# Kernel optimization log

Measured on AMD Instinct MI355X. Metric: run time of the kernel, lower is better.

The kernel has to match this reference:

```python
import jax, jax.numpy as jnp
import numpy as np

B, S, D, H = 2, 1024, 768, 12
HD = D // H          # head_dim = 64
DFF = 4 * D          # 3072
EPS = 1e-5


def _ln(x, g, b):
    m = x.mean(-1, keepdims=True)
    v = ((x - m) ** 2).mean(-1, keepdims=True)
    return (x - m) * jax.lax.rsqrt(v + EPS) * g + b


def setup_inputs() -> dict:
    key = jax.random.key(0)
    ks = jax.random.split(key, 8)
    w = lambda k, shape: jax.random.normal(k, shape, jnp.float32) * 0.02
    return {
        "inp": jax.random.normal(ks[0], (B, S, D), jnp.float32),
        "attention_mask": jnp.zeros((B, S), bool),  # True = masked out (filled with -inf)
        "rel_matrix": jax.random.randint(ks[1], (B, S, S), -1, 2, jnp.int32),  # values in {-1,0,1}
        "qkv_w": w(ks[2], (3 * D, D)),
        "rel_A": w(ks[3], (3, HD)),        # relative_position_emb_A.weight
        "o_w": w(ks[4], (D, D)),
        "w1": w(ks[5], (DFF, D)), "b1": jnp.zeros((DFF,), jnp.float32),
        "w2": w(ks[6], (D, DFF)), "b2": jnp.zeros((D,), jnp.float32),
        "ln1_g": jnp.ones((D,), jnp.float32), "ln1_b": jnp.zeros((D,), jnp.float32),
        "ln2_g": jnp.ones((D,), jnp.float32), "ln2_b": jnp.zeros((D,), jnp.float32),
    }


def reference(inp, attention_mask, rel_matrix, qkv_w, rel_A, o_w,
              w1, b1, w2, b2, ln1_g, ln1_b, ln2_g, ln2_b):
    x = _ln(inp, ln1_g, ln1_b)
    qkv = x @ qkv_w.T                                  # (B,S,3D)
    q, k, v = jnp.split(qkv, 3, axis=-1)
    heads = lambda t: t.reshape(B, S, H, HD).transpose(0, 2, 1, 3)  # (B,H,S,HD)
    q, k, v = heads(q), heads(k), heads(v)

    # q @ (k + rel_emb)^T without materializing k_aug:
    # q.k^T term plus per-(q,key) relative term gathered from q @ A^T.
    logits = jnp.einsum("bhqd,bhkd->bhqk", q, k)       # (B,H,S,S)
    r = jnp.einsum("bhqd,cd->bhqc", q, rel_A)          # (B,H,S,3)
    idx = (rel_matrix + 1).astype(jnp.int32)           # (B,S,S) in {0,1,2}
    rel = jnp.take_along_axis(r, jnp.broadcast_to(idx[:, None], (B, H, S, S)), axis=-1)
    logits = (logits + rel) / np.sqrt(HD).astype(np.float32)
    # masked_fill: -inf where mask is True
    logits = jnp.where(attention_mask[:, None, None, :], -jnp.inf, logits)

    attn = jax.nn.softmax(logits, axis=-1)
    out = jnp.einsum("bhqk,bhkd->bhqd", attn, v)
    out = out.transpose(0, 2, 1, 3).reshape(B, S, D)
    inp = inp + out @ o_w.T                            # residual (dropout=0)

    h = _ln(inp, ln2_g, ln2_b)
    mlp = jax.nn.relu(h @ w1.T + b1) @ w2.T + b2
    return inp + mlp
```

## Files before the change

kernel.cpp:

```cpp
#include <hip/hip_runtime.h>
#include <hip/hip_bf16.h>

#define BB 2
#define SS 1024
#define DD 768
#define HH 12
#define HD 64
#define DFF 3072
#define EPS 1e-5f
#define BS2 (BB * SS)
#define BSD ((size_t)BS2 * DD)

typedef unsigned short ushort_t;
typedef unsigned char uchar_t;
using short8 = __attribute__((ext_vector_type(8))) short;
using f32x4  = __attribute__((ext_vector_type(4))) float;

__device__ __forceinline__ ushort_t f2bf_rne(float f) {
    union { float f; unsigned u; } x; x.f = f;
    unsigned r = x.u + 0x7fff + ((x.u >> 16) & 1);
    return (ushort_t)(r >> 16);
}
__device__ __forceinline__ float bf2f(short u) {
    union { unsigned i; float f; } x;
    x.i = ((unsigned)(ushort_t)u) << 16;
    return x.f;
}

__global__ __launch_bounds__(256) void cvt_bf16(
    const float* __restrict__ in, ushort_t* __restrict__ out, int n4)
{
    int i = blockIdx.x * 256 + threadIdx.x;
    if (i < n4) {
        float4 v = ((const float4*)in)[i];
        ushort4 o;
        o.x = f2bf_rne(v.x); o.y = f2bf_rne(v.y);
        o.z = f2bf_rne(v.z); o.w = f2bf_rne(v.w);
        ((ushort4*)out)[i] = o;
    }
}

__global__ __launch_bounds__(256) void build_codes(
    const int* __restrict__ rel, const uchar_t* __restrict__ mask,
    unsigned* __restrict__ codes)
{
    int tid = blockIdx.x * 256 + threadIdx.x;
    int l15 = tid & 15;
    int kt  = (tid >> 4) & 15;
    int q   = (tid >> 8) & (SS - 1);
    int b   = tid >> 18;
    const int* rrow = rel + ((size_t)(b * SS + q)) * SS + kt * 64 + l15;
    const uchar_t* mrow = mask + (size_t)b * SS + kt * 64 + l15;
    unsigned o = 0;
#pragma unroll
    for (int nt = 0; nt < 4; ++nt) {
        unsigned c = mrow[nt * 16] ? 3u : (unsigned)(rrow[nt * 16] + 1);
        o |= c << (8 * nt);
    }
    codes[((size_t)(b * SS + q) * 16 + kt) * 16 + l15] = o;
}

__global__ __launch_bounds__(256) void ln_kernel_bf(
    const float* __restrict__ x, const float* __restrict__ g,
    const float* __restrict__ b, ushort_t* __restrict__ y)
{
    const int row = blockIdx.x;
    const float* xr = x + (size_t)row * DD;
    float s = 0.f, ss = 0.f;
    for (int i = threadIdx.x; i < DD; i += 256) {
        float v = xr[i];
        s += v; ss += v * v;
    }
    for (int off = 32; off; off >>= 1) {
        s  += __shfl_down(s,  off);
        ss += __shfl_down(ss, off);
    }
    __shared__ float reds[4], redss[4], bc[2];
    int t = threadIdx.x;
    if ((t & 63) == 0) { reds[t >> 6] = s; redss[t >> 6] = ss; }
    __syncthreads();
    if (t == 0) {
        float S1 = reds[0] + reds[1] + reds[2] + reds[3];
        float S2 = redss[0] + redss[1] + redss[2] + redss[3];
        float mean = S1 / DD;
        float var = S2 / DD - mean * mean;
        bc[0] = mean;
        bc[1] = rsqrtf(var + EPS);
    }
    __syncthreads();
    float mean = bc[0], inv = bc[1];
    ushort_t* yr = y + (size_t)row * DD;
    for (int i = threadIdx.x; i < DD; i += 256) {
        yr[i] = f2bf_rne((xr[i] - mean) * inv * g[i] + b[i]);
    }
}

template <int Z, bool HAS_BIAS>
__global__ __launch_bounds__(256) void merge_partials(
    const float* __restrict__ part, const float* __restrict__ base,
    const float* __restrict__ bias, float* __restrict__ outp, int n4)
{
    int i = blockIdx.x * 256 + threadIdx.x;
    if (i >= n4) return;
    float4 v = ((const float4*)base)[i];
    if (HAS_BIAS) {
        int col4 = (i * 4) % DD;
        float4 bv = *(const float4*)(bias + col4);
        v.x += bv.x; v.y += bv.y; v.z += bv.z; v.w += bv.w;
    }
#pragma unroll
    for (int z = 0; z < Z; ++z) {
        float4 pz = ((const float4*)(part + (size_t)z * BSD))[i];
        v.x += pz.x; v.y += pz.y; v.z += pz.z; v.w += pz.w;
    }
    ((float4*)outp)[i] = v;
}

template <bool RELU, bool OUT_BF16, bool HAS_BIAS, bool PARTIAL>
__global__ __launch_bounds__(256) void gemm_tile(
    const ushort_t* __restrict__ A, const ushort_t* __restrict__ W,
    const float* __restrict__ bias, void* __restrict__ Cout,
    int M, int N, int K, int Ksplit)
{
    __shared__ __align__(16) ushort_t As[512 * 8];
    __shared__ __align__(16) ushort_t Bs[256 * 8];

    const int t  = threadIdx.x;
    const int n0 = blockIdx.x * 64;
    const int m0 = blockIdx.y * 128;
    const int kb = blockIdx.z * Ksplit;
    const int w  = t >> 6;
    const int l  = t & 63;
    const int wm = (w & 1) * 64;
    const int wn = (w >> 1) * 32;
    const int l15  = l & 15;
    const int quad = l >> 4;

    const ushort_t* gA0 = A + (size_t)(m0 + (t & 127)) * K + kb + (t >> 7) * 8;
    const ushort_t* gA1 = gA0 + 16;
    const ushort_t* gB0 = W + (size_t)(n0 + (t & 63)) * K + kb + (t >> 6) * 8;
    ushort_t* lA0 = &As[(size_t)t * 8];
    ushort_t* lA1 = &As[(size_t)(t + 256) * 8];
    ushort_t* lB0 = &Bs[(size_t)t * 8];

    const ushort_t* aptr = &As[(size_t)(quad * 128 + wm + l15) * 8];
    const ushort_t* bptr = &Bs[(size_t)(quad * 64 + wn + l15) * 8];

    f32x4 acc[4][2] = {};

    for (int k0 = 0; k0 < Ksplit; k0 += 32) {
        __syncthreads();
        __builtin_amdgcn_global_load_lds(
            (const __attribute__((address_space(1))) unsigned int*)(gA0 + k0),
            (__attribute__((address_space(3))) unsigned int*)lA0, 16, 0, 0);
        __builtin_amdgcn_global_load_lds(
            (const __attribute__((address_space(1))) unsigned int*)(gA1 + k0),
            (__attribute__((address_space(3))) unsigned int*)lA1, 16, 0, 0);
        __builtin_amdgcn_global_load_lds(
            (const __attribute__((address_space(1))) unsigned int*)(gB0 + k0),
            (__attribute__((address_space(3))) unsigned int*)lB0, 16, 0, 0);
        __syncthreads();

        short8 af[4], bf[2];
#pragma unroll
        for (int i = 0; i < 4; ++i)
            af[i] = *(const short8*)(aptr + (size_t)i * 16 * 8);
#pragma unroll
        for (int j = 0; j < 2; ++j)
            bf[j] = *(const short8*)(bptr + (size_t)j * 16 * 8);
#pragma unroll
        for (int i = 0; i < 4; ++i)
#pragma unroll
            for (int j = 0; j < 2; ++j)
                acc[i][j] = __builtin_amdgcn_mfma_f32_16x16x32_bf16(
                    af[i], bf[j], acc[i][j], 0, 0, 0);
    }

    if (PARTIAL) {
        float* Cp = (float*)Cout + (size_t)blockIdx.z * ((size_t)M * N);
#pragma unroll
        for (int i = 0; i < 4; ++i) {
            const int row = m0 + wm + i * 16 + quad * 4;
#pragma unroll
            for (int j = 0; j < 2; ++j) {
                const int col = n0 + wn + j * 16 + l15;
#pragma unroll
                for (int r = 0; r < 4; ++r)
                    Cp[(size_t)(row + r) * N + col] = acc[i][j][r];
            }
        }
    } else {
#pragma unroll
        for (int i = 0; i < 4; ++i) {
            const int row = m0 + wm + i * 16 + quad * 4;
#pragma unroll
            for (int j = 0; j < 2; ++j) {
                const int col = n0 + wn + j * 16 + l15;
                const float bv = HAS_BIAS ? bias[col] : 0.f;
#pragma unroll
                for (int r = 0; r < 4; ++r) {
                    float v = acc[i][j][r] + bv;
                    if (RELU) v = fmaxf(v, 0.f);
                    if (OUT_BF16)
                        ((ushort_t*)Cout)[(size_t)(row + r) * N + col] = f2bf_rne(v);
                    else
                        ((float*)Cout)[(size_t)(row + r) * N + col] = v;
                }
            }
        }
    }
}

__global__ __launch_bounds__(256) void attn_mfma_kernel(
    const ushort_t* __restrict__ qkv,
    const unsigned* __restrict__ codes,
    const float* __restrict__ rel_A,
    float* __restrict__ Opart,
    float* __restrict__ lpart)
{
    __shared__ __align__(16) ushort_t Ks[64 * 64];
    __shared__ __align__(16) unsigned Vt2[64 * 36];
    __shared__ __align__(16) ushort_t Ps[64 * 72];
    __shared__ __align__(16) float r3s[64][4];

    const int bx = blockIdx.x;
    const int ks = bx & 3;
    const int qt = (bx >> 2) & 15;
    const int h  = (bx >> 6) % HH;
    const int b  = bx / (64 * HH);
    const int q0 = qt * 64;
    const int t  = threadIdx.x;
    const int w  = t >> 6;
    const int l  = t & 63;
    const int l15  = l & 15;
    const int quad = l >> 4;

    const size_t qrow = (size_t)(b * SS + q0 + w * 16 + l15) * (3 * DD) + h * HD;
    const short8 qf0 = *(const short8*)(qkv + qrow + quad * 8);
    const short8 qf1 = *(const short8*)(qkv + qrow + 32 + quad * 8);

    {
        float rv[3];
#pragma unroll
        for (int c = 0; c < 3; ++c) {
            const float* a = rel_A + c * HD + quad * 8;
            float acc = 0.f;
#pragma unroll
            for (int j = 0; j < 8; ++j) acc += bf2f(qf0[j]) * a[j];
#pragma unroll
            for (int j = 0; j < 8; ++j) acc += bf2f(qf1[j]) * a[32 + j];
            acc += __shfl_xor(acc, 16);
            acc += __shfl_xor(acc, 32);
            rv[c] = acc;
        }
        if (quad == 0) {
            float4 f4 = make_float4(rv[0], rv[1], rv[2], -2.4e31f);
            *(float4*)&r3s[w * 16 + l15][0] = f4;
        }
    }
    __syncthreads();
    float4 r3v[4];
#pragma unroll
    for (int reg = 0; reg < 4; ++reg)
        r3v[reg] = *(const float4*)&r3s[w * 16 + quad * 4 + reg][0];

    float l_run[4] = {0.f, 0.f, 0.f, 0.f};
    f32x4 oacc[4] = {};

    for (int kt = ks * 4; kt < ks * 4 + 4; ++kt) {
        const int k0 = kt * 64;
        __syncthreads();
        {
            const int r  = t >> 3;
            const int cp = t & 7;
            const int cl  = cp ^ (r & 7);
            const ushort_t* g = qkv + (size_t)(b * SS + k0 + r) * (3 * DD) + DD + h * HD + cl * 8;
            __builtin_amdgcn_global_load_lds(
                (const __attribute__((address_space(1))) unsigned*)g,
                (__attribute__((address_space(3))) unsigned*)(Ks + (size_t)t * 8), 16, 0, 0);
            const int r2  = r + 32;
            const int cl2 = cp ^ (r2 & 7);
            const ushort_t* g2 = qkv + (size_t)(b * SS + k0 + r2) * (3 * DD) + DD + h * HD + cl2 * 8;
            __builtin_amdgcn_global_load_lds(
                (const __attribute__((address_space(1))) unsigned*)g2,
                (__attribute__((address_space(3))) unsigned*)(Ks + (size_t)(t + 256) * 8), 16, 0, 0);
        }
        {
            const int kp = t >> 3;
            const int dg = t & 7;
            const ushort_t* g = qkv + (size_t)(b * SS + k0 + 2 * kp) * (3 * DD) + 2 * DD + h * HD + dg * 8;
            short8 va = *(const short8*)g;
            short8 vb = *(const short8*)(g + 3 * DD);
            const int kps = kp ^ ((dg & 7) * 4);
#pragma unroll
            for (int i = 0; i < 8; ++i)
                Vt2[(size_t)(dg * 8 + i) * 36 + kps] =
                    (unsigned)(ushort_t)va[i] | ((unsigned)(ushort_t)vb[i] << 16);
        }
        __syncthreads();

        f32x4 sacc[4] = {};
#pragma unroll
        for (int kc = 0; kc < 2; ++kc) {
            const short8 qv = kc ? qf1 : qf0;
#pragma unroll
            for (int nt = 0; nt < 4; ++nt) {
                const int row = nt * 16 + l15;
                const int cp  = (kc * 4 + quad) ^ (row & 7);
                const short8 kf = *(const short8*)(Ks + (size_t)row * 64 + cp * 8);
                sacc[nt] = __builtin_amdgcn_mfma_f32_16x16x32_bf16(qv, kf, sacc[nt], 0, 0, 0);
            }
        }

#pragma unroll
        for (int reg = 0; reg < 4; ++reg) {
            const int qloc = w * 16 + quad * 4 + reg;
            const unsigned cds = codes[((size_t)(b * SS + q0 + qloc) * 16 + kt) * 16 + l15];
            const float4 r4 = r3v[reg];
#pragma unroll
            for (int nt = 0; nt < 4; ++nt) {
                const unsigned c = (cds >> (8 * nt)) & 0xff;
                float rvv = (c == 0) ? r4.x : (c == 1) ? r4.y : (c == 2) ? r4.z : r4.w;
                const float p = __expf((sacc[nt][reg] + rvv) * 0.125f);
                l_run[reg] += p;
                Ps[(size_t)qloc * 72 + nt * 16 + l15] = f2bf_rne(p);
            }
        }

#pragma unroll
        for (int kc = 0; kc < 2; ++kc) {
            const short8 pf = *(const short8*)(Ps + (size_t)(w * 16 + l15) * 72 + kc * 32 + quad * 8);
#pragma unroll
            for (int dt = 0; dt < 4; ++dt) {
                const int d  = dt * 16 + l15;
                const int dg = d >> 3;
                const int kps0 = (kc * 16 + quad * 4) ^ ((dg & 7) * 4);
                const short8 vf = *(const short8*)((const ushort_t*)&Vt2[(size_t)d * 36 + kps0]);
                oacc[dt] = __builtin_amdgcn_mfma_f32_16x16x32_bf16(pf, vf, oacc[dt], 0, 0, 0);
            }
        }
    }

    float* Op = Opart + (size_t)ks * BSD;
    float* lp = lpart + (size_t)ks * BS2 * HH;
#pragma unroll
    for (int reg = 0; reg < 4; ++reg) {
        float ls = l_run[reg];
        ls += __shfl_xor(ls, 1);
        ls += __shfl_xor(ls, 2);
        ls += __shfl_xor(ls, 4);
        ls += __shfl_xor(ls, 8);
        const int orow = b * SS + q0 + w * 16 + quad * 4 + reg;
#pragma unroll
        for (int dt = 0; dt < 4; ++dt)
            Op[(size_t)orow * DD + h * HD + dt * 16 + l15] = oacc[dt][reg];
        if (l15 == 0) lp[(size_t)orow * HH + h] = ls;
    }
}

__global__ __launch_bounds__(256) void attn_merge(
    const float* __restrict__ Opart, const float* __restrict__ lpart,
    ushort_t* __restrict__ att_bf)
{
    int i = blockIdx.x * 256 + threadIdx.x;
    int row = (i * 4) / DD;
    int h   = ((i * 4) % DD) >> 6;
    float lsum = 0.f;
#pragma unroll
    for (int z = 0; z < 4; ++z)
        lsum += lpart[(size_t)z * BS2 * HH + (size_t)row * HH + h];
    float inv = 1.0f / lsum;
    float4 os = ((const float4*)Opart)[i];
#pragma unroll
    for (int z = 1; z < 4; ++z) {
        float4 oz = ((const float4*)(Opart + (size_t)z * BSD))[i];
        os.x += oz.x; os.y += oz.y; os.z += oz.z; os.w += oz.w;
    }
    ushort4 o;
    o.x = f2bf_rne(os.x * inv);
    o.y = f2bf_rne(os.y * inv);
    o.z = f2bf_rne(os.z * inv);
    o.w = f2bf_rne(os.w * inv);
    ((ushort4*)att_bf)[i] = o;
}

extern "C" void kernel_launch(void* const* d_in, const int* in_sizes, int n_in,
                              void* d_out, int out_size, void* d_ws, size_t ws_size,
                              hipStream_t stream) {
    const float* inp   = (const float*)d_in[0];
    const uchar_t* amask = (const uchar_t*)d_in[1];
    const int*   relm  = (const int*)d_in[2];
    const float* qkv_w = (const float*)d_in[3];
    const float* rel_A = (const float*)d_in[4];
    const float* o_w   = (const float*)d_in[5];
    const float* w1    = (const float*)d_in[6];
    const float* b1    = (const float*)d_in[7];
    const float* w2    = (const float*)d_in[8];
    const float* b2    = (const float*)d_in[9];
    const float* ln1_g = (const float*)d_in[10];
    const float* ln1_b = (const float*)d_in[11];
    const float* ln2_g = (const float*)d_in[12];
    const float* ln2_b = (const float*)d_in[13];
    float* out = (float*)d_out;

    char* p = (char*)d_ws;
    ushort_t* x_bf   = (ushort_t*)p; p += BSD * 2;
    ushort_t* att_bf = (ushort_t*)p; p += BSD * 2;
    ushort_t* h_bf   = (ushort_t*)p; p += BSD * 2;
    ushort_t* ff_bf  = (ushort_t*)p; p += (size_t)BS2 * DFF * 2;
    ushort_t* qkvw_bf= (ushort_t*)p; p += (size_t)3 * DD * DD * 2;
    ushort_t* ow_bf  = (ushort_t*)p; p += (size_t)DD * DD * 2;
    ushort_t* w1_bf  = (ushort_t*)p; p += (size_t)DFF * DD * 2;
    ushort_t* w2_bf  = (ushort_t*)p; p += (size_t)DD * DFF * 2;
    ushort_t* qkv_bf = (ushort_t*)p; p += (size_t)BS2 * 3 * DD * 2;
    float*    resid  = (float*)p;    p += BSD * 4;
    float*    pool   = (float*)p;    p += 4 * BSD * 4;
    float*    lpart  = (float*)p;    p += (size_t)4 * BS2 * HH * 4;
    unsigned* codes  = (unsigned*)p; p += (size_t)BB * SS * SS;

    {
        int n4;
        n4 = 3 * DD * DD / 4;
        cvt_bf16<<<(n4 + 255) / 256, 256, 0, stream>>>(qkv_w, qkvw_bf, n4);
        n4 = DD * DD / 4;
        cvt_bf16<<<(n4 + 255) / 256, 256, 0, stream>>>(o_w, ow_bf, n4);
        n4 = DFF * DD / 4;
        cvt_bf16<<<(n4 + 255) / 256, 256, 0, stream>>>(w1, w1_bf, n4);
        cvt_bf16<<<(n4 + 255) / 256, 256, 0, stream>>>(w2, w2_bf, n4);
        build_codes<<<(BB * SS * 256) / 256, 256, 0, stream>>>(relm, amask, codes);
    }

    ln_kernel_bf<<<BS2, 256, 0, stream>>>(inp, ln1_g, ln1_b, x_bf);

    gemm_tile<false, true, false, false>
        <<<dim3(3 * DD / 64, BS2 / 128, 1), 256, 0, stream>>>(
        x_bf, qkvw_bf, nullptr, qkv_bf, BS2, 3 * DD, DD, DD);

    attn_mfma_kernel<<<BB * HH * 16 * 4, 256, 0, stream>>>(
        qkv_bf, codes, rel_A, pool, lpart);
    attn_merge<<<(int)(BSD / 4 / 256), 256, 0, stream>>>(pool, lpart, att_bf);

    gemm_tile<false, false, false, true>
        <<<dim3(DD / 64, BS2 / 128, 2), 256, 0, stream>>>(
        att_bf, ow_bf, nullptr, pool, BS2, DD, DD, DD / 2);
    merge_partials<2, false><<<(int)(BSD / 4 / 256), 256, 0, stream>>>(
        pool, inp, nullptr, resid, (int)(BSD / 4));

    ln_kernel_bf<<<BS2, 256, 0, stream>>>(resid, ln2_g, ln2_b, h_bf);

    gemm_tile<true, true, true, false>
        <<<dim3(DFF / 64, BS2 / 128, 1), 256, 0, stream>>>(
        h_bf, w1_bf, b1, ff_bf, BS2, DFF, DD, DD);

    gemm_tile<false, false, false, true>
        <<<dim3(DD / 64, BS2 / 128, 4), 256, 0, stream>>>(
        ff_bf, w2_bf, nullptr, pool, BS2, DD, DFF, DFF / 4);
    merge_partials<4, true><<<(int)(BSD / 4 / 256), 256, 0, stream>>>(
        pool, resid, b2, out, (int)(BSD / 4));
}
```

Baseline: 278.3 us.

## Fuse weight conversions, merge residual with LN2, and double GEMM K-step

Replaces the four per-weight bf16 conversion launches with a single kernel that writes into the contiguous bf16 weight buffer. Fuses the two-way split-K merge plus residual add with the second LayerNorm, so the residual is not re-read by a separate kernel. Widens the GEMM tile K-step from 32 to 64, doubling the shared-memory tiles, to halve the number of barrier pairs per K loop at the cost of more LDS per block.

New measurement: 275.3 us. About the same (-1.1%).

```diff
diff --git a/kernel.cpp b/kernel.cpp
--- a/kernel.cpp
+++ b/kernel.cpp
@@ -27,17 +27,28 @@
     return x.f;
 }
 
-__global__ __launch_bounds__(256) void cvt_bf16(
-    const float* __restrict__ in, ushort_t* __restrict__ out, int n4)
+#define CVT_N1 (3 * DD * DD / 4)
+#define CVT_N2 (CVT_N1 + DD * DD / 4)
+#define CVT_N3 (CVT_N2 + DFF * DD / 4)
+#define CVT_NT (CVT_N3 + DD * DFF / 4)
+
+__global__ __launch_bounds__(256) void cvt_all(
+    const float* __restrict__ qkv_w, const float* __restrict__ o_w,
+    const float* __restrict__ w1, const float* __restrict__ w2,
+    ushort_t* __restrict__ dst)
 {
     int i = blockIdx.x * 256 + threadIdx.x;
-    if (i < n4) {
-        float4 v = ((const float4*)in)[i];
-        ushort4 o;
-        o.x = f2bf_rne(v.x); o.y = f2bf_rne(v.y);
-        o.z = f2bf_rne(v.z); o.w = f2bf_rne(v.w);
-        ((ushort4*)out)[i] = o;
-    }
+    if (i >= CVT_NT) return;
+    const float* src; int off;
+    if (i < CVT_N1)      { src = qkv_w; off = i; }
+    else if (i < CVT_N2) { src = o_w;   off = i - CVT_N1; }
+    else if (i < CVT_N3) { src = w1;    off = i - CVT_N2; }
+    else                 { src = w2;    off = i - CVT_N3; }
+    float4 v = ((const float4*)src)[off];
+    ushort4 o;
+    o.x = f2bf_rne(v.x); o.y = f2bf_rne(v.y);
+    o.z = f2bf_rne(v.z); o.w = f2bf_rne(v.w);
+    ((ushort4*)dst)[i] = o;
 }
 
 __global__ __launch_bounds__(256) void build_codes(
@@ -95,21 +106,66 @@
     }
 }
 
-template <int Z, bool HAS_BIAS>
-__global__ __launch_bounds__(256) void merge_partials(
-    const float* __restrict__ part, const float* __restrict__ base,
-    const float* __restrict__ bias, float* __restrict__ outp, int n4)
+__global__ __launch_bounds__(256) void merge2_ln_kernel(
+    const float* __restrict__ part, const float* __restrict__ inp,
+    const float* __restrict__ g, const float* __restrict__ b,
+    float* __restrict__ resid, ushort_t* __restrict__ h_bf)
+{
+    const int row = blockIdx.x;
+    const int t = threadIdx.x;
+    float4 v = make_float4(0.f, 0.f, 0.f, 0.f);
+    const size_t idx = (size_t)row * (DD / 4) + t;
+    if (t < DD / 4) {
+        v = ((const float4*)inp)[idx];
+        float4 p0 = ((const float4*)part)[idx];
+        float4 p1 = ((const float4*)(part + BSD))[idx];
+        v.x += p0.x + p1.x; v.y += p0.y + p1.y;
+        v.z += p0.z + p1.z; v.w += p0.w + p1.w;
+        ((float4*)resid)[idx] = v;
+    }
+    float s  = v.x + v.y + v.z + v.w;
+    float ss = v.x * v.x + v.y * v.y + v.z * v.z + v.w * v.w;
+    for (int off = 32; off; off >>= 1) {
+        s  += __shfl_down(s,  off);
+        ss += __shfl_down(ss, off);
+    }
+    __shared__ float reds[4], redss[4], bc[2];
+    if ((t & 63) == 0) { reds[t >> 6] = s; redss[t >> 6] = ss; }
+    __syncthreads();
+    if (t == 0) {
+        float S1 = reds[0] + reds[1] + reds[2] + reds[3];
+        float S2 = redss[0] + redss[1] + redss[2] + redss[3];
+        float mean = S1 / DD;
+        float var = S2 / DD - mean * mean;
+        bc[0] = mean;
+        bc[1] = rsqrtf(var + EPS);
+    }
+    __syncthreads();
+    if (t < DD / 4) {
+        const float mean = bc[0], inv = bc[1];
+        float4 gv = ((const float4*)g)[t];
+        float4 bv = ((const float4*)b)[t];
+        ushort4 o;
+        o.x = f2bf_rne((v.x - mean) * inv * gv.x + bv.x);
+        o.y = f2bf_rne((v.y - mean) * inv * gv.y + bv.y);
+        o.z = f2bf_rne((v.z - mean) * inv * gv.z + bv.z);
+        o.w = f2bf_rne((v.w - mean) * inv * gv.w + bv.w);
+        ((ushort4*)h_bf)[idx] = o;
+    }
+}
+
+__global__ __launch_bounds__(256) void merge4_kernel(
+    const float* __restrict__ part, const float* __restrict__ resid,
+    const float* __restrict__ b2, float* __restrict__ outp, int n4)
 {
     int i = blockIdx.x * 256 + threadIdx.x;
     if (i >= n4) return;
-    float4 v = ((const float4*)base)[i];
-    if (HAS_BIAS) {
-        int col4 = (i * 4) % DD;
-        float4 bv = *(const float4*)(bias + col4);
-        v.x += bv.x; v.y += bv.y; v.z += bv.z; v.w += bv.w;
-    }
-#pragma unroll
-    for (int z = 0; z < Z; ++z) {
+    float4 v = ((const float4*)resid)[i];
+    int col4 = (i * 4) % DD;
+    float4 bv = *(const float4*)(b2 + col4);
+    v.x += bv.x; v.y += bv.y; v.z += bv.z; v.w += bv.w;
+#pragma unroll
+    for (int z = 0; z < 4; ++z) {
         float4 pz = ((const float4*)(part + (size_t)z * BSD))[i];
         v.x += pz.x; v.y += pz.y; v.z += pz.z; v.w += pz.w;
     }
@@ -122,8 +178,8 @@
     const float* __restrict__ bias, void* __restrict__ Cout,
     int M, int N, int K, int Ksplit)
 {
-    __shared__ __align__(16) ushort_t As[512 * 8];
-    __shared__ __align__(16) ushort_t Bs[256 * 8];
+    __shared__ __align__(16) ushort_t As[1024 * 8];
+    __shared__ __align__(16) ushort_t Bs[512 * 8];
 
     const int t  = threadIdx.x;
     const int n0 = blockIdx.x * 64;
@@ -136,44 +192,47 @@
     const int l15  = l & 15;
     const int quad = l >> 4;
 
-    const ushort_t* gA0 = A + (size_t)(m0 + (t & 127)) * K + kb + (t >> 7) * 8;
-    const ushort_t* gA1 = gA0 + 16;
-    const ushort_t* gB0 = W + (size_t)(n0 + (t & 63)) * K + kb + (t >> 6) * 8;
-    ushort_t* lA0 = &As[(size_t)t * 8];
-    ushort_t* lA1 = &As[(size_t)(t + 256) * 8];
-    ushort_t* lB0 = &Bs[(size_t)t * 8];
-
-    const ushort_t* aptr = &As[(size_t)(quad * 128 + wm + l15) * 8];
-    const ushort_t* bptr = &Bs[(size_t)(quad * 64 + wn + l15) * 8];
+    const ushort_t* gA = A + (size_t)(m0 + (t & 127)) * K + kb + (t >> 7) * 8;
+    ushort_t* lA = &As[(size_t)t * 8];
+    const ushort_t* gB = W + (size_t)(n0 + (t & 63)) * K + kb + (t >> 6) * 8;
+    ushort_t* lB = &Bs[(size_t)t * 8];
 
     f32x4 acc[4][2] = {};
 
-    for (int k0 = 0; k0 < Ksplit; k0 += 32) {
+    for (int k0 = 0; k0 < Ksplit; k0 += 64) {
         __syncthreads();
-        __builtin_amdgcn_global_load_lds(
-            (const __attribute__((address_space(1))) unsigned int*)(gA0 + k0),
-            (__attribute__((address_space(3))) unsigned int*)lA0, 16, 0, 0);
-        __builtin_amdgcn_global_load_lds(
-            (const __attribute__((address_space(1))) unsigned int*)(gA1 + k0),
-            (__attribute__((address_space(3))) unsigned int*)lA1, 16, 0, 0);
-        __builtin_amdgcn_global_load_lds(
-            (const __attribute__((address_space(1))) unsigned int*)(gB0 + k0),
-            (__attribute__((address_space(3))) unsigned int*)lB0, 16, 0, 0);
+#pragma unroll
+        for (int ii = 0; ii < 4; ++ii)
+            __builtin_amdgcn_global_load_lds(
+                (const __attribute__((address_space(1))) unsigned int*)(gA + k0 + ii * 16),
+                (__attribute__((address_space(3))) unsigned int*)(lA + (size_t)ii * 256 * 8),
+                16, 0, 0);
+#pragma unroll
+        for (int ii = 0; ii < 2; ++ii)
+            __builtin_amdgcn_global_load_lds(
+                (const __attribute__((address_space(1))) unsigned int*)(gB + k0 + ii * 32),
+                (__attribute__((address_space(3))) unsigned int*)(lB + (size_t)ii * 256 * 8),
+                16, 0, 0);
         __syncthreads();
 
-        short8 af[4], bf[2];
-#pragma unroll
-        for (int i = 0; i < 4; ++i)
-            af[i] = *(const short8*)(aptr + (size_t)i * 16 * 8);
-#pragma unroll
-        for (int j = 0; j < 2; ++j)
-            bf[j] = *(const short8*)(bptr + (size_t)j * 16 * 8);
-#pragma unroll
-        for (int i = 0; i < 4; ++i)
+#pragma unroll
+        for (int ks = 0; ks < 2; ++ks) {
+            const ushort_t* aptr = &As[(size_t)((ks * 4 + quad) * 128 + wm + l15) * 8];
+            const ushort_t* bptr = &Bs[(size_t)((ks * 4 + quad) * 64 + wn + l15) * 8];
+            short8 af[4], bf[2];
+#pragma unroll
+            for (int i = 0; i < 4; ++i)
+                af[i] = *(const short8*)(aptr + (size_t)i * 16 * 8);
 #pragma unroll
             for (int j = 0; j < 2; ++j)
-                acc[i][j] = __builtin_amdgcn_mfma_f32_16x16x32_bf16(
-                    af[i], bf[j], acc[i][j], 0, 0, 0);
+                bf[j] = *(const short8*)(bptr + (size_t)j * 16 * 8);
+#pragma unroll
+            for (int i = 0; i < 4; ++i)
+#pragma unroll
+                for (int j = 0; j < 2; ++j)
+                    acc[i][j] = __builtin_amdgcn_mfma_f32_16x16x32_bf16(
+                        af[i], bf[j], acc[i][j], 0, 0, 0);
+        }
     }
 
     if (PARTIAL) {
@@ -418,17 +477,8 @@
     float*    lpart  = (float*)p;    p += (size_t)4 * BS2 * HH * 4;
     unsigned* codes  = (unsigned*)p; p += (size_t)BB * SS * SS;
 
-    {
-        int n4;
-        n4 = 3 * DD * DD / 4;
-        cvt_bf16<<<(n4 + 255) / 256, 256, 0, stream>>>(qkv_w, qkvw_bf, n4);
-        n4 = DD * DD / 4;
-        cvt_bf16<<<(n4 + 255) / 256, 256, 0, stream>>>(o_w, ow_bf, n4);
-        n4 = DFF * DD / 4;
-        cvt_bf16<<<(n4 + 255) / 256, 256, 0, stream>>>(w1, w1_bf, n4);
-        cvt_bf16<<<(n4 + 255) / 256, 256, 0, stream>>>(w2, w2_bf, n4);
-        build_codes<<<(BB * SS * 256) / 256, 256, 0, stream>>>(relm, amask, codes);
-    }
+    cvt_all<<<(CVT_NT + 255) / 256, 256, 0, stream>>>(qkv_w, o_w, w1, w2, qkvw_bf);
+    build_codes<<<(BB * SS * 256) / 256, 256, 0, stream>>>(relm, amask, codes);
 
     ln_kernel_bf<<<BS2, 256, 0, stream>>>(inp, ln1_g, ln1_b, x_bf);
 
@@ -443,10 +493,9 @@
     gemm_tile<false, false, false, true>
         <<<dim3(DD / 64, BS2 / 128, 2), 256, 0, stream>>>(
         att_bf, ow_bf, nullptr, pool, BS2, DD, DD, DD / 2);
-    merge_partials<2, false><<<(int)(BSD / 4 / 256), 256, 0, stream>>>(
-        pool, inp, nullptr, resid, (int)(BSD / 4));
-
-    ln_kernel_bf<<<BS2, 256, 0, stream>>>(resid, ln2_g, ln2_b, h_bf);
+
+    merge2_ln_kernel<<<BS2, 256, 0, stream>>>(
+        pool, inp, ln2_g, ln2_b, resid, h_bf);
 
     gemm_tile<true, true, true, false>
         <<<dim3(DFF / 64, BS2 / 128, 1), 256, 0, stream>>>(
@@ -455,6 +504,7 @@
     gemm_tile<false, false, false, true>
         <<<dim3(DD / 64, BS2 / 128, 4), 256, 0, stream>>>(
         ff_bf, w2_bf, nullptr, pool, BS2, DD, DFF, DFF / 4);
-    merge_partials<4, true><<<(int)(BSD / 4 / 256), 256, 0, stream>>>(
+
+    merge4_kernel<<<(int)(BSD / 4 / 256), 256, 0, stream>>>(
         pool, resid, b2, out, (int)(BSD / 4));
 }
```
